# Optimization experiments

Hardware: AMD Instinct MI355X
Metric: run time of the kernel (lower is better)

Reference implementation:

```python
import jax, jax.numpy as jnp
import numpy as np

TEMP = 0.5
ALPHA = 1.0
BETA = 5.5
GAMMA = 5.0
N, D, C, M = 400, 512, 1000, 16000


def _normalize(x, axis=-1, eps=1e-12):
    return x / jnp.maximum(jnp.linalg.norm(x, axis=axis, keepdims=True), eps)


def _scale(x, target):
    # min-max scale x into the value range of target (global scalars)
    y = (x - x.min()) / (x.max() - x.min())
    y = y * (target.max() - target.min())
    y = y + target.min()
    return y


def setup_inputs() -> dict:
    key = jax.random.key(0)
    k1, k2, k3, k4 = jax.random.split(key, 4)
    image_features = jax.random.normal(k1, (N, D), dtype=jnp.float32)
    text_embeds = jax.random.normal(k2, (C, D), dtype=jnp.float32)
    support_feats = _normalize(jax.random.normal(k3, (D, M), dtype=jnp.float32), axis=0)
    support_labels = jax.random.randint(k4, (M,), 0, C)
    return {
        "image_features": image_features,
        "text_embeds": text_embeds,
        "support_feats": support_feats,
        "support_labels": support_labels,
    }


def reference(image_features, text_embeds, support_feats, support_labels):
    # one-hot support targets [M, C]
    support_targets = jax.nn.one_hot(support_labels, C, dtype=jnp.float32)

    # L2-normalize features (forward() normalizes both text and image features)
    text_features = _normalize(text_embeds, axis=-1).T          # [D, C]
    img = _normalize(image_features, axis=-1)                   # [N, D]

    # class distributions via temperature softmax
    train_logits = (support_feats.T @ text_features) / TEMP     # [M, C]
    test_logits = (img @ text_features) / TEMP                  # [N, C]
    train_log_dist = jax.nn.log_softmax(train_logits, axis=-1)  # log q  [M, C]
    test_log_dist = jax.nn.log_softmax(test_logits, axis=-1)    # log p  [N, C]
    test_dist = jnp.exp(test_log_dist)                          # p      [N, C]

    # KL(p_i || q_j) = sum_c p_ic log p_ic - sum_c p_ic log q_jc  -> one GEMM
    entropy_term = jnp.sum(test_dist * test_log_dist, axis=-1, keepdims=True)  # [N, 1]
    kl_divs = entropy_term - test_dist @ train_log_dist.T                      # [N, M]

    clip_logits = 100.0 * (img @ text_features)                 # [N, C]
    new_knowledge = img @ support_feats                         # [N, M]

    neg_affs = _scale(kl_divs, new_knowledge)                   # [N, M]
    affinities = -neg_affs
    kl_logits = affinities @ support_targets                    # [N, C]
    cache_logits = jnp.exp(-(BETA - BETA * new_knowledge)) @ support_targets  # [N, C]

    tipx_logits = clip_logits + kl_logits * GAMMA + cache_logits * ALPHA
    return tipx_logits
```

## Files before the change

kernel.cpp:

```cpp
#include <hip/hip_runtime.h>
#include <math.h>

#define TEMP_F   0.5f
#define ALPHA_F  1.0f
#define BETA_F   5.5f
#define GAMMA_F  5.0f
#define N_IMG    400
#define D_DIM    512
#define C_CLS    1000
#define C_PAD    1024
#define M_SUP    16000

typedef __attribute__((ext_vector_type(8))) short short8;
typedef __attribute__((ext_vector_type(4))) short short4v;
typedef __attribute__((ext_vector_type(4))) float f32x4;

__device__ __forceinline__ short f2bf(float f) {
    unsigned u = __float_as_uint(f);
    unsigned r = (u + 0x7fffu + ((u >> 16) & 1u)) >> 16;
    return (short)r;
}
__device__ __forceinline__ float bf2f(short s) {
    return __uint_as_float(((unsigned)(unsigned short)s) << 16);
}
__device__ __forceinline__ unsigned encf(float f) {
    unsigned u = __float_as_uint(f);
    return (u & 0x80000000u) ? ~u : (u | 0x80000000u);
}
__device__ __forceinline__ float decf(unsigned u) {
    return (u & 0x80000000u) ? __uint_as_float(u & 0x7FFFFFFFu) : __uint_as_float(~u);
}

__device__ __forceinline__ float block_reduce_sum(float v) {
    __shared__ float red[4];
    #pragma unroll
    for (int o = 32; o > 0; o >>= 1) v += __shfl_down(v, o, 64);
    int w = threadIdx.x >> 6, l = threadIdx.x & 63;
    __syncthreads();
    if (l == 0) red[w] = v;
    __syncthreads();
    float r = red[0];
    int nw = blockDim.x >> 6;
    for (int i = 1; i < nw; ++i) r += red[i];
    return r;
}

__device__ __forceinline__ void gload_lds16(const void* g, void* l) {
    __builtin_amdgcn_global_load_lds(
        (const __attribute__((address_space(1))) unsigned int*)g,
        (__attribute__((address_space(3))) unsigned int*)l, 16, 0, 0);
}

template<int EPI>
__device__ __forceinline__ void gemm_body(
    const short* __restrict__ A, const short* __restrict__ B, void* __restrict__ Cm,
    int I, int Jclamp, int Jout, int K, long lda, long ldb, long ldc, float alpha,
    const float* __restrict__ ent, const float* __restrict__ lse,
    unsigned* __restrict__ mm, float* __restrict__ out2,
    int i0, int j0, short (*As)[4096], short (*Bs)[4096])
{
    const int tid = threadIdx.x;
    const int wave = tid >> 6;
    const int lane = tid & 63;

    const int srow = wave * 16 + (lane >> 2);
    const int skk  = (lane & 3) * 8;

    const int wm = (wave & 1) * 64;
    const int wn = (wave >> 1) * 64;
    const int fr = lane & 15;
    const int fq = lane >> 4;

    f32x4 acc[4][4] = {};

    auto stage = [&](int buf, int k0) {
        #pragma unroll
        for (int q = 0; q < 2; ++q) {
            int gi = i0 + q * 64 + srow; if (gi > I - 1) gi = I - 1;
            gload_lds16(A + (long)gi * lda + k0 + skk, As[buf] + q * 2048 + wave * 512);
        }
        #pragma unroll
        for (int q = 0; q < 2; ++q) {
            int gj = j0 + q * 64 + srow; if (gj > Jclamp - 1) gj = Jclamp - 1;
            gload_lds16(B + (long)gj * ldb + k0 + skk, Bs[buf] + q * 2048 + wave * 512);
        }
    };

    const int nt = K >> 5;
    stage(0, 0);
    if (nt > 1) stage(1, 32);
    if (nt > 2) stage(2, 64);

    for (int t = 0; t < nt; ++t) {
        const int b = t % 3;

        if (t + 2 < nt)      asm volatile("s_waitcnt vmcnt(8)" ::: "memory");
        else if (t + 1 < nt) asm volatile("s_waitcnt vmcnt(4)" ::: "memory");
        else                 asm volatile("s_waitcnt vmcnt(0)" ::: "memory");
        __builtin_amdgcn_s_barrier();
        __builtin_amdgcn_sched_barrier(0);

        short8 af[4], bfr[4];
        #pragma unroll
        for (int mi = 0; mi < 4; ++mi)
            af[mi] = *(const short8*)(As[b] + (wm + mi * 16 + fr) * 32 + fq * 8);
        #pragma unroll
        for (int ni = 0; ni < 4; ++ni)
            bfr[ni] = *(const short8*)(Bs[b] + (wn + ni * 16 + fr) * 32 + fq * 8);

        asm volatile("s_waitcnt lgkmcnt(0)" ::: "memory");
        __builtin_amdgcn_sched_barrier(0);
        __builtin_amdgcn_s_barrier();

        if (t + 3 < nt) stage(b, (t + 3) << 5);

        __builtin_amdgcn_s_setprio(1);
        #pragma unroll
        for (int mi = 0; mi < 4; ++mi)
            #pragma unroll
            for (int ni = 0; ni < 4; ++ni)
                acc[mi][ni] = __builtin_amdgcn_mfma_f32_16x16x32_bf16(
                    af[mi], bfr[ni], acc[mi][ni], 0, 0, 0);
        __builtin_amdgcn_s_setprio(0);
    }

    float lmin = INFINITY, lmax = -INFINITY;

    #pragma unroll
    for (int mi = 0; mi < 4; ++mi) {
        #pragma unroll
        for (int ni = 0; ni < 4; ++ni) {
            int gj = j0 + wn + ni * 16 + fr;
            float lsev = 0.f;
            if (EPI == 2) lsev = lse[gj < Jout ? gj : (Jout - 1)];
            #pragma unroll
            for (int t = 0; t < 4; ++t) {
                int gi = i0 + wm + mi * 16 + fq * 4 + t;
                float v = alpha * acc[mi][ni][t];
                if (EPI == 2) {
                    int gic = gi < I ? gi : (I - 1);
                    v = ent[gic] - v + lsev;
                }
                if (EPI == 2 || EPI == 3) { lmin = fminf(lmin, v); lmax = fmaxf(lmax, v); }
                if (gi < I && gj < Jout) {
                    if (EPI == 1) ((short*)Cm)[(long)gi * ldc + gj] = f2bf(v);
                    else          ((float*)Cm)[(long)gi * ldc + gj] = v;
                }
                if (EPI == 4 && gi < I && gj < C_CLS)
                    out2[(long)gi * C_CLS + gj] = 100.f * v;
            }
        }
    }

    if (EPI == 2 || EPI == 3) {
        #pragma unroll
        for (int o = 32; o > 0; o >>= 1) {
            lmin = fminf(lmin, __shfl_down(lmin, o, 64));
            lmax = fmaxf(lmax, __shfl_down(lmax, o, 64));
        }
        __shared__ float rmin[4], rmax[4];
        if (lane == 0) { rmin[wave] = lmin; rmax[wave] = lmax; }
        __syncthreads();
        if (tid == 0) {
            float bmin = fminf(fminf(rmin[0], rmin[1]), fminf(rmin[2], rmin[3]));
            float bmax = fmaxf(fmaxf(rmax[0], rmax[1]), fmaxf(rmax[2], rmax[3]));
            const int base = (EPI == 2) ? 0 : 2;
            atomicMin(&mm[base + 0], encf(bmin));
            atomicMax(&mm[base + 1], encf(bmax));
        }
    }
}


__global__ __launch_bounds__(256) void prep_k(
    const float* __restrict__ text_embeds, const float* __restrict__ image_features,
    const float* __restrict__ S,
    short* __restrict__ Tnb, short* __restrict__ imgb, short* __restrict__ Sb,
    unsigned* __restrict__ mm)
{
    const int b = blockIdx.x;
    if (b == 0 && threadIdx.x < 4)
        mm[threadIdx.x] = (threadIdx.x & 1) ? encf(-INFINITY) : encf(INFINITY);

    if (b < 1400) {
        const float* s;
        short* d;
        if (b < 1000) { s = text_embeds + (long)b * D_DIM;            d = Tnb  + (long)b * D_DIM; }
        else          { s = image_features + (long)(b - 1000) * D_DIM; d = imgb + (long)(b - 1000) * D_DIM; }
        float ss = 0.f;
        for (int c = threadIdx.x; c < D_DIM; c += 256) { float v = s[c]; ss += v * v; }
        float tot = block_reduce_sum(ss);
        float inv = 1.0f / fmaxf(sqrtf(tot), 1e-12f);
        for (int c = threadIdx.x; c < D_DIM; c += 256) d[c] = f2bf(s[c] * inv);
    } else {
        __shared__ float tile[64][65];
        int l = b - 1400;
        int m0 = (l % 250) * 64, d0 = (l / 250) * 64;
        int ml = (threadIdx.x & 15) * 4;
        int dl = threadIdx.x >> 4;
        #pragma unroll
        for (int r = 0; r < 64; r += 16) {
            f32x4 v = *(const f32x4*)(S + (long)(d0 + dl + r) * M_SUP + m0 + ml);
            tile[dl + r][ml + 0] = v[0];
            tile[dl + r][ml + 1] = v[1];
            tile[dl + r][ml + 2] = v[2];
            tile[dl + r][ml + 3] = v[3];
        }
        __syncthreads();
        int mw = threadIdx.x >> 4;
        int dc = (threadIdx.x & 15) * 4;
        #pragma unroll
        for (int r = 0; r < 64; r += 16) {
            short4v o;
            #pragma unroll
            for (int k = 0; k < 4; ++k) o[k] = f2bf(tile[dc + k][mw + r]);
            *(short4v*)(Sb + (long)(m0 + mw + r) * D_DIM + d0 + dc) = o;
        }
    }
}

__global__ __launch_bounds__(256) void mega_gemm_k(
    const short* __restrict__ Sb, const short* __restrict__ Tnb,
    const short* __restrict__ imgb,
    short* __restrict__ tb, float* __restrict__ nk, float* __restrict__ dot,
    unsigned* __restrict__ mm, float* __restrict__ out)
{
    __shared__ short As[3][4096];
    __shared__ short Bs[3][4096];
    const int lin = blockIdx.x;

    if (lin < 1000) {
        int gt = (lin & 7) * 125 + (lin >> 3);
        int i0 = (gt >> 3) * 128;
        int j0 = (gt & 7) * 128;
        gemm_body<1>(Sb, Tnb, tb, M_SUP, C_CLS, C_PAD, D_DIM, D_DIM, D_DIM, C_PAD,
                     2.0f, nullptr, nullptr, nullptr, nullptr, i0, j0, As, Bs);
    } else if (lin < 1512) {
        int l = lin - 1000;
        int xcd = l & 7;
        int idx = l >> 3;
        int i0 = (idx & 3) * 128;
        int j0 = (xcd * 16 + (idx >> 2)) * 128;
        gemm_body<3>(imgb, Sb, nk, N_IMG, M_SUP, M_SUP, D_DIM, D_DIM, D_DIM, M_SUP,
                     1.0f, nullptr, nullptr, mm, nullptr, i0, j0, As, Bs);
    } else {
        int l = lin - 1512;
        int i0 = (l >> 3) * 128;
        int j0 = (l & 7) * 128;
        gemm_body<4>(imgb, Tnb, dot, N_IMG, C_CLS, C_PAD, D_DIM, D_DIM, D_DIM, C_PAD,
                     1.0f, nullptr, nullptr, nullptr, out, i0, j0, As, Bs);
    }
}

__global__ void lse_softmax_k(
    const short* __restrict__ tb, float* __restrict__ lse,
    const float* __restrict__ dot, short* __restrict__ pb, float* __restrict__ ent)
{
    const int b = blockIdx.x;
    const int lane = threadIdx.x & 63;
    if (b < 4000) {
        int row = b * 4 + (threadIdx.x >> 6);
        const short* r = tb + (long)row * C_PAD;
        short8 v0 = *(const short8*)(r + lane * 8);
        short8 v1 = *(const short8*)(r + 512 + lane * 8);
        bool act1 = lane < 61;
        float f0[8], f1[8];
        float mx = -INFINITY;
        #pragma unroll
        for (int j = 0; j < 8; ++j) { f0[j] = bf2f(v0[j]); mx = fmaxf(mx, f0[j]); }
        if (act1) {
            #pragma unroll
            for (int j = 0; j < 8; ++j) { f1[j] = bf2f(v1[j]); mx = fmaxf(mx, f1[j]); }
        }
        #pragma unroll
        for (int o = 32; o > 0; o >>= 1) mx = fmaxf(mx, __shfl_xor(mx, o, 64));
        float se = 0.f;
        #pragma unroll
        for (int j = 0; j < 8; ++j) se += __expf(f0[j] - mx);
        if (act1) {
            #pragma unroll
            for (int j = 0; j < 8; ++j) se += __expf(f1[j] - mx);
        }
        #pragma unroll
        for (int o = 32; o > 0; o >>= 1) se += __shfl_xor(se, o, 64);
        if (lane == 0) lse[row] = mx + __logf(se);
    } else {
        int n = (b - 4000) * 4 + (threadIdx.x >> 6);
        const float* dr = dot + (long)n * C_PAD;
        short* pr = pb + (long)n * C_PAD;
        f32x4 v[4];
        #pragma unroll
        for (int pp = 0; pp < 4; ++pp)
            v[pp] = *(const f32x4*)(dr + pp * 256 + lane * 4);
        float mx = -INFINITY;
        #pragma unroll
        for (int pp = 0; pp < 4; ++pp) {
            bool valid = (pp < 3) || (lane < 58);
            if (valid)
                #pragma unroll
                for (int j = 0; j < 4; ++j) mx = fmaxf(mx, 2.f * v[pp][j]);
        }
        #pragma unroll
        for (int o = 32; o > 0; o >>= 1) mx = fmaxf(mx, __shfl_xor(mx, o, 64));
        float se = 0.f;
        #pragma unroll
        for (int pp = 0; pp < 4; ++pp) {
            bool valid = (pp < 3) || (lane < 58);
            if (valid)
                #pragma unroll
                for (int j = 0; j < 4; ++j) se += __expf(2.f * v[pp][j] - mx);
        }
        #pragma unroll
        for (int o = 32; o > 0; o >>= 1) se += __shfl_xor(se, o, 64);
        float logsum = mx + __logf(se);
        float e = 0.f;
        #pragma unroll
        for (int pp = 0; pp < 4; ++pp) {
            bool valid = (pp < 3) || (lane < 58);
            short4v o4;
            #pragma unroll
            for (int j = 0; j < 4; ++j) {
                if (valid) {
                    float lp = 2.f * v[pp][j] - logsum;
                    float pv = __expf(lp);
                    o4[j] = f2bf(pv);
                    e += pv * lp;
                } else {
                    o4[j] = 0;
                }
            }
            *(short4v*)(pr + pp * 256 + lane * 4) = o4;
        }
        #pragma unroll
        for (int o = 32; o > 0; o >>= 1) e += __shfl_xor(e, o, 64);
        if (lane == 0) ent[n] = e;
    }
}

__global__ __launch_bounds__(256) void gemm2_k(
    const short* __restrict__ pb, const short* __restrict__ tb, float* __restrict__ kl,
    const float* __restrict__ ent, const float* __restrict__ lse,
    unsigned* __restrict__ mm)
{
    __shared__ short As[3][4096];
    __shared__ short Bs[3][4096];
    int lin = blockIdx.x;
    int xcd = lin & 7;
    int idx = lin >> 3;
    int i0 = (idx & 3) * 128;
    int j0 = (xcd * 16 + (idx >> 2)) * 128;
    gemm_body<2>(pb, tb, kl, N_IMG, M_SUP, M_SUP, C_PAD, C_PAD, C_PAD, M_SUP,
                 1.0f, ent, lse, mm, nullptr, i0, j0, As, Bs);
}

__global__ __launch_bounds__(256) void final_partial_k(
    const float* __restrict__ kl, const float* __restrict__ nk,
    const int* __restrict__ labels, const unsigned* __restrict__ mm,
    float* __restrict__ out)
{
    int n = blockIdx.x;
    int q = blockIdx.y;
    __shared__ float bins[C_CLS];
    for (int c = threadIdx.x; c < C_CLS; c += 256) bins[c] = 0.f;
    __syncthreads();
    float klmin = decf(mm[0]), klmax = decf(mm[1]);
    float nkmin = decf(mm[2]), nkmax = decf(mm[3]);
    float ratio = (nkmax - nkmin) / (klmax - klmin);
    const int m0 = q * (M_SUP / 4);
    const float4* kl4 = (const float4*)(kl + (long)n * M_SUP + m0);
    const float4* nk4 = (const float4*)(nk + (long)n * M_SUP + m0);
    const int4*  lb4 = (const int4*)(labels + m0);
    const int nv = M_SUP / 4 / 4;
    for (int v = threadIdx.x; v < nv; v += 256) {
        float4 kv = kl4[v];
        float4 vv = nk4[v];
        int4   lv = lb4[v];
        float y, contrib;
        y = (kv.x - klmin) * ratio + nkmin;
        contrib = -GAMMA_F * y + ALPHA_F * __expf(BETA_F * (vv.x - 1.0f));
        atomicAdd(&bins[lv.x], contrib);
        y = (kv.y - klmin) * ratio + nkmin;
        contrib = -GAMMA_F * y + ALPHA_F * __expf(BETA_F * (vv.y - 1.0f));
        atomicAdd(&bins[lv.y], contrib);
        y = (kv.z - klmin) * ratio + nkmin;
        contrib = -GAMMA_F * y + ALPHA_F * __expf(BETA_F * (vv.z - 1.0f));
        atomicAdd(&bins[lv.z], contrib);
        y = (kv.w - klmin) * ratio + nkmin;
        contrib = -GAMMA_F * y + ALPHA_F * __expf(BETA_F * (vv.w - 1.0f));
        atomicAdd(&bins[lv.w], contrib);
    }
    __syncthreads();
    for (int c = threadIdx.x; c < C_CLS; c += 256)
        atomicAdd(&out[(long)n * C_CLS + c], bins[c]);
}

extern "C" void kernel_launch(void* const* d_in, const int* in_sizes, int n_in,
                              void* d_out, int out_size, void* d_ws, size_t ws_size,
                              hipStream_t stream) {
    const float* image_features = (const float*)d_in[0];
    const float* text_embeds    = (const float*)d_in[1];
    const float* support_feats  = (const float*)d_in[2];
    const int*   support_labels = (const int*)d_in[3];
    float* out = (float*)d_out;

    char* base = (char*)d_ws;
    size_t off = 0;
    auto alloc = [&](size_t bytes) {
        void* p = base + off;
        off = (off + bytes + 255) & ~(size_t)255;
        return p;
    };
    short* Tnb  = (short*)alloc(sizeof(short) * C_CLS * D_DIM);
    short* imgb = (short*)alloc(sizeof(short) * N_IMG * D_DIM);
    short* Sb   = (short*)alloc(sizeof(short) * M_SUP * D_DIM);
    short* tb   = (short*)alloc(sizeof(short) * M_SUP * C_PAD);
    short* pb   = (short*)alloc(sizeof(short) * N_IMG * C_PAD);
    float* dot  = (float*)alloc(sizeof(float) * N_IMG * C_PAD);
    float* lse  = (float*)alloc(sizeof(float) * M_SUP);
    float* ent  = (float*)alloc(sizeof(float) * N_IMG);
    float* kl   = (float*)alloc(sizeof(float) * N_IMG * M_SUP);
    float* nk   = (float*)alloc(sizeof(float) * N_IMG * M_SUP);
    unsigned* mm = (unsigned*)alloc(256);

    prep_k<<<3400, 256, 0, stream>>>(
        text_embeds, image_features, support_feats, Tnb, imgb, Sb, mm);

    mega_gemm_k<<<1544, 256, 0, stream>>>(Sb, Tnb, imgb, tb, nk, dot, mm, out);

    lse_softmax_k<<<4100, 256, 0, stream>>>(tb, lse, dot, pb, ent);

    gemm2_k<<<512, 256, 0, stream>>>(pb, tb, kl, ent, lse, mm);

    final_partial_k<<<dim3(N_IMG, 4), 256, 0, stream>>>(kl, nk, support_labels, mm, out);
}
```

Measured before the change: 211.4 us.

## Reassociate KL GEMM through text features and fuse train logsumexp into GEMM epilogue

Rather than writing the full [M,C] train-logit matrix and running a K=1024 GEMM against it, the code reassociates p @ (S^T T)^T as (p @ T^T) @ S. It computes a small [N,D] intermediate W and then a K=512 GEMM against the support features. Per-row sum-exp of the train logits is accumulated with atomics in the first GEMM's epilogue, and the log is taken in the KL epilogue, so the bf16 train-logit buffer and the separate LSE pass go away. The sum-exp is taken without max subtraction, which is only safe because the logits are bounded (cosine times 2). It also adds a transposed text copy, an extra tiny GEMM launch, and a second bf16 rounding of W.

```diff
diff --git a/kernel.cpp b/kernel.cpp
--- a/kernel.cpp
+++ b/kernel.cpp
@@ -124,6 +124,40 @@
         __builtin_amdgcn_s_setprio(0);
     }
 
+    if (EPI == 5) {
+        float rs[4][4];
+        #pragma unroll
+        for (int mi = 0; mi < 4; ++mi)
+            #pragma unroll
+            for (int t = 0; t < 4; ++t) rs[mi][t] = 0.f;
+        #pragma unroll
+        for (int mi = 0; mi < 4; ++mi)
+            #pragma unroll
+            for (int ni = 0; ni < 4; ++ni) {
+                int gj = j0 + wn + ni * 16 + fr;
+                if (gj < Jout) {
+                    #pragma unroll
+                    for (int t = 0; t < 4; ++t)
+                        rs[mi][t] += __expf(alpha * acc[mi][ni][t]);
+                }
+            }
+        #pragma unroll
+        for (int o = 1; o <= 8; o <<= 1)
+            #pragma unroll
+            for (int mi = 0; mi < 4; ++mi)
+                #pragma unroll
+                for (int t = 0; t < 4; ++t)
+                    rs[mi][t] += __shfl_xor(rs[mi][t], o, 64);
+        if ((lane & 15) == 0) {
+            #pragma unroll
+            for (int mi = 0; mi < 4; ++mi)
+                #pragma unroll
+                for (int t = 0; t < 4; ++t)
+                    atomicAdd(out2 + (i0 + wm + mi * 16 + fq * 4 + t), rs[mi][t]);
+        }
+        return;
+    }
+
     float lmin = INFINITY, lmax = -INFINITY;
 
     #pragma unroll
@@ -132,7 +166,7 @@
         for (int ni = 0; ni < 4; ++ni) {
             int gj = j0 + wn + ni * 16 + fr;
             float lsev = 0.f;
-            if (EPI == 2) lsev = lse[gj < Jout ? gj : (Jout - 1)];
+            if (EPI == 2) lsev = __logf(lse[gj < Jout ? gj : (Jout - 1)]);
             #pragma unroll
             for (int t = 0; t < 4; ++t) {
                 int gi = i0 + wm + mi * 16 + fq * 4 + t;
@@ -175,24 +209,37 @@
 __global__ __launch_bounds__(256) void prep_k(
     const float* __restrict__ text_embeds, const float* __restrict__ image_features,
     const float* __restrict__ S,
-    short* __restrict__ Tnb, short* __restrict__ imgb, short* __restrict__ Sb,
-    unsigned* __restrict__ mm)
+    short* __restrict__ Tnb, short* __restrict__ TnT, short* __restrict__ imgb,
+    short* __restrict__ Sb, float* __restrict__ se, unsigned* __restrict__ mm)
 {
     const int b = blockIdx.x;
     if (b == 0 && threadIdx.x < 4)
         mm[threadIdx.x] = (threadIdx.x & 1) ? encf(-INFINITY) : encf(INFINITY);
 
-    if (b < 1400) {
-        const float* s;
-        short* d;
-        if (b < 1000) { s = text_embeds + (long)b * D_DIM;            d = Tnb  + (long)b * D_DIM; }
-        else          { s = image_features + (long)(b - 1000) * D_DIM; d = imgb + (long)(b - 1000) * D_DIM; }
+    if (b < 1000) {
+        const float* s = text_embeds + (long)b * D_DIM;
+        short* d = Tnb + (long)b * D_DIM;
+        float ss = 0.f;
+        for (int c = threadIdx.x; c < D_DIM; c += 256) { float v = s[c]; ss += v * v; }
+        float tot = block_reduce_sum(ss);
+        float inv = 1.0f / fmaxf(sqrtf(tot), 1e-12f);
+        for (int c = threadIdx.x; c < D_DIM; c += 256) {
+            short bv = f2bf(s[c] * inv);
+            d[c] = bv;
+            TnT[(long)c * C_PAD + b] = bv;
+        }
+        if (b < 24)
+            for (int f = threadIdx.x; f < D_DIM; f += 256)
+                TnT[(long)f * C_PAD + 1000 + b] = 0;
+    } else if (b < 1400) {
+        const float* s = image_features + (long)(b - 1000) * D_DIM;
+        short* d = imgb + (long)(b - 1000) * D_DIM;
         float ss = 0.f;
         for (int c = threadIdx.x; c < D_DIM; c += 256) { float v = s[c]; ss += v * v; }
         float tot = block_reduce_sum(ss);
         float inv = 1.0f / fmaxf(sqrtf(tot), 1e-12f);
         for (int c = threadIdx.x; c < D_DIM; c += 256) d[c] = f2bf(s[c] * inv);
-    } else {
+    } else if (b < 3400) {
         __shared__ float tile[64][65];
         int l = b - 1400;
         int m0 = (l % 250) * 64, d0 = (l / 250) * 64;
@@ -216,13 +263,16 @@
             for (int k = 0; k < 4; ++k) o[k] = f2bf(tile[dc + k][mw + r]);
             *(short4v*)(Sb + (long)(m0 + mw + r) * D_DIM + d0 + dc) = o;
         }
+    } else {
+        int base = (b - 3400) * 1000;
+        for (int i = threadIdx.x; i < 1000; i += 256) se[base + i] = 0.f;
     }
 }
 
 __global__ __launch_bounds__(256) void mega_gemm_k(
     const short* __restrict__ Sb, const short* __restrict__ Tnb,
     const short* __restrict__ imgb,
-    short* __restrict__ tb, float* __restrict__ nk, float* __restrict__ dot,
+    float* __restrict__ se, float* __restrict__ nk, float* __restrict__ dot,
     unsigned* __restrict__ mm, float* __restrict__ out)
 {
     __shared__ short As[3][4096];
@@ -233,8 +283,8 @@
         int gt = (lin & 7) * 125 + (lin >> 3);
         int i0 = (gt >> 3) * 128;
         int j0 = (gt & 7) * 128;
-        gemm_body<1>(Sb, Tnb, tb, M_SUP, C_CLS, C_PAD, D_DIM, D_DIM, D_DIM, C_PAD,
-                     2.0f, nullptr, nullptr, nullptr, nullptr, i0, j0, As, Bs);
+        gemm_body<5>(Sb, Tnb, nullptr, M_SUP, C_CLS, C_CLS, D_DIM, D_DIM, D_DIM, 0,
+                     2.0f, nullptr, nullptr, nullptr, se, i0, j0, As, Bs);
     } else if (lin < 1512) {
         int l = lin - 1000;
         int xcd = l & 7;
@@ -252,94 +302,76 @@
     }
 }
 
-__global__ void lse_softmax_k(
-    const short* __restrict__ tb, float* __restrict__ lse,
-    const float* __restrict__ dot, short* __restrict__ pb, float* __restrict__ ent)
-{
-    const int b = blockIdx.x;
+__global__ void softmax_k(const float* __restrict__ dot, short* __restrict__ pb,
+                          float* __restrict__ ent)
+{
     const int lane = threadIdx.x & 63;
-    if (b < 4000) {
-        int row = b * 4 + (threadIdx.x >> 6);
-        const short* r = tb + (long)row * C_PAD;
-        short8 v0 = *(const short8*)(r + lane * 8);
-        short8 v1 = *(const short8*)(r + 512 + lane * 8);
-        bool act1 = lane < 61;
-        float f0[8], f1[8];
-        float mx = -INFINITY;
-        #pragma unroll
-        for (int j = 0; j < 8; ++j) { f0[j] = bf2f(v0[j]); mx = fmaxf(mx, f0[j]); }
-        if (act1) {
-            #pragma unroll
-            for (int j = 0; j < 8; ++j) { f1[j] = bf2f(v1[j]); mx = fmaxf(mx, f1[j]); }
-        }
-        #pragma unroll
-        for (int o = 32; o > 0; o >>= 1) mx = fmaxf(mx, __shfl_xor(mx, o, 64));
-        float se = 0.f;
-        #pragma unroll
-        for (int j = 0; j < 8; ++j) se += __expf(f0[j] - mx);
-        if (act1) {
-            #pragma unroll
-            for (int j = 0; j < 8; ++j) se += __expf(f1[j] - mx);
-        }
-        #pragma unroll
-        for (int o = 32; o > 0; o >>= 1) se += __shfl_xor(se, o, 64);
-        if (lane == 0) lse[row] = mx + __logf(se);
-    } else {
-        int n = (b - 4000) * 4 + (threadIdx.x >> 6);
-        const float* dr = dot + (long)n * C_PAD;
-        short* pr = pb + (long)n * C_PAD;
-        f32x4 v[4];
-        #pragma unroll
-        for (int pp = 0; pp < 4; ++pp)
-            v[pp] = *(const f32x4*)(dr + pp * 256 + lane * 4);
-        float mx = -INFINITY;
-        #pragma unroll
-        for (int pp = 0; pp < 4; ++pp) {
-            bool valid = (pp < 3) || (lane < 58);
-            if (valid)
-                #pragma unroll
-                for (int j = 0; j < 4; ++j) mx = fmaxf(mx, 2.f * v[pp][j]);
-        }
-        #pragma unroll
-        for (int o = 32; o > 0; o >>= 1) mx = fmaxf(mx, __shfl_xor(mx, o, 64));
-        float se = 0.f;
-        #pragma unroll
-        for (int pp = 0; pp < 4; ++pp) {
-            bool valid = (pp < 3) || (lane < 58);
-            if (valid)
-                #pragma unroll
-                for (int j = 0; j < 4; ++j) se += __expf(2.f * v[pp][j] - mx);
-        }
-        #pragma unroll
-        for (int o = 32; o > 0; o >>= 1) se += __shfl_xor(se, o, 64);
-        float logsum = mx + __logf(se);
-        float e = 0.f;
-        #pragma unroll
-        for (int pp = 0; pp < 4; ++pp) {
-            bool valid = (pp < 3) || (lane < 58);
-            short4v o4;
-            #pragma unroll
-            for (int j = 0; j < 4; ++j) {
-                if (valid) {
-                    float lp = 2.f * v[pp][j] - logsum;
-                    float pv = __expf(lp);
-                    o4[j] = f2bf(pv);
-                    e += pv * lp;
-                } else {
-                    o4[j] = 0;
-                }
+    int n = blockIdx.x * 4 + (threadIdx.x >> 6);
+    const float* dr = dot + (long)n * C_PAD;
+    short* pr = pb + (long)n * C_PAD;
+    f32x4 v[4];
+    #pragma unroll
+    for (int pp = 0; pp < 4; ++pp)
+        v[pp] = *(const f32x4*)(dr + pp * 256 + lane * 4);
+    float mx = -INFINITY;
+    #pragma unroll
+    for (int pp = 0; pp < 4; ++pp) {
+        bool valid = (pp < 3) || (lane < 58);
+        if (valid)
+            #pragma unroll
+            for (int j = 0; j < 4; ++j) mx = fmaxf(mx, 2.f * v[pp][j]);
+    }
+    #pragma unroll
+    for (int o = 32; o > 0; o >>= 1) mx = fmaxf(mx, __shfl_xor(mx, o, 64));
+    float se = 0.f;
+    #pragma unroll
+    for (int pp = 0; pp < 4; ++pp) {
+        bool valid = (pp < 3) || (lane < 58);
+        if (valid)
+            #pragma unroll
+            for (int j = 0; j < 4; ++j) se += __expf(2.f * v[pp][j] - mx);
+    }
+    #pragma unroll
+    for (int o = 32; o > 0; o >>= 1) se += __shfl_xor(se, o, 64);
+    float logsum = mx + __logf(se);
+    float e = 0.f;
+    #pragma unroll
+    for (int pp = 0; pp < 4; ++pp) {
+        bool valid = (pp < 3) || (lane < 58);
+        short4v o4;
+        #pragma unroll
+        for (int j = 0; j < 4; ++j) {
+            if (valid) {
+                float lp = 2.f * v[pp][j] - logsum;
+                float pv = __expf(lp);
+                o4[j] = f2bf(pv);
+                e += pv * lp;
+            } else {
+                o4[j] = 0;
             }
-            *(short4v*)(pr + pp * 256 + lane * 4) = o4;
-        }
-        #pragma unroll
-        for (int o = 32; o > 0; o >>= 1) e += __shfl_xor(e, o, 64);
-        if (lane == 0) ent[n] = e;
-    }
-}
-
-__global__ __launch_bounds__(256) void gemm2_k(
-    const short* __restrict__ pb, const short* __restrict__ tb, float* __restrict__ kl,
-    const float* __restrict__ ent, const float* __restrict__ lse,
+        }
+        *(short4v*)(pr + pp * 256 + lane * 4) = o4;
+    }
+    #pragma unroll
+    for (int o = 32; o > 0; o >>= 1) e += __shfl_xor(e, o, 64);
+    if (lane == 0) ent[n] = e;
+}
+
+__global__ __launch_bounds__(256) void wgemm_k(
+    const short* __restrict__ pb, const short* __restrict__ TnT,
+    short* __restrict__ Wb)
+{
+    __shared__ short As[3][4096];
+    __shared__ short Bs[3][4096];
+    int i0 = (blockIdx.x >> 2) * 128;
+    int j0 = (blockIdx.x & 3) * 128;
+    gemm_body<1>(pb, TnT, Wb, N_IMG, D_DIM, D_DIM, C_PAD, C_PAD, C_PAD, D_DIM,
+                 2.0f, nullptr, nullptr, nullptr, nullptr, i0, j0, As, Bs);
+}
+
+__global__ __launch_bounds__(256) void qgemm_k(
+    const short* __restrict__ Wb, const short* __restrict__ Sb, float* __restrict__ kl,
+    const float* __restrict__ ent, const float* __restrict__ se,
     unsigned* __restrict__ mm)
 {
     __shared__ short As[3][4096];
@@ -349,8 +381,8 @@
     int idx = lin >> 3;
     int i0 = (idx & 3) * 128;
     int j0 = (xcd * 16 + (idx >> 2)) * 128;
-    gemm_body<2>(pb, tb, kl, N_IMG, M_SUP, M_SUP, C_PAD, C_PAD, C_PAD, M_SUP,
-                 1.0f, ent, lse, mm, nullptr, i0, j0, As, Bs);
+    gemm_body<2>(Wb, Sb, kl, N_IMG, M_SUP, M_SUP, D_DIM, D_DIM, D_DIM, M_SUP,
+                 1.0f, ent, se, mm, nullptr, i0, j0, As, Bs);
 }
 
 __global__ __launch_bounds__(256) void final_partial_k(
@@ -411,25 +443,28 @@
         return p;
     };
     short* Tnb  = (short*)alloc(sizeof(short) * C_CLS * D_DIM);
+    short* TnT  = (short*)alloc(sizeof(short) * D_DIM * C_PAD);
     short* imgb = (short*)alloc(sizeof(short) * N_IMG * D_DIM);
     short* Sb   = (short*)alloc(sizeof(short) * M_SUP * D_DIM);
-    short* tb   = (short*)alloc(sizeof(short) * M_SUP * C_PAD);
     short* pb   = (short*)alloc(sizeof(short) * N_IMG * C_PAD);
+    short* Wb   = (short*)alloc(sizeof(short) * N_IMG * D_DIM);
     float* dot  = (float*)alloc(sizeof(float) * N_IMG * C_PAD);
-    float* lse  = (float*)alloc(sizeof(float) * M_SUP);
+    float* se   = (float*)alloc(sizeof(float) * M_SUP);
     float* ent  = (float*)alloc(sizeof(float) * N_IMG);
     float* kl   = (float*)alloc(sizeof(float) * N_IMG * M_SUP);
     float* nk   = (float*)alloc(sizeof(float) * N_IMG * M_SUP);
     unsigned* mm = (unsigned*)alloc(256);
 
-    prep_k<<<3400, 256, 0, stream>>>(
-        text_embeds, image_features, support_feats, Tnb, imgb, Sb, mm);
-
-    mega_gemm_k<<<1544, 256, 0, stream>>>(Sb, Tnb, imgb, tb, nk, dot, mm, out);
-
-    lse_softmax_k<<<4100, 256, 0, stream>>>(tb, lse, dot, pb, ent);
-
-    gemm2_k<<<512, 256, 0, stream>>>(pb, tb, kl, ent, lse, mm);
+    prep_k<<<3416, 256, 0, stream>>>(
+        text_embeds, image_features, support_feats, Tnb, TnT, imgb, Sb, se, mm);
+
+    mega_gemm_k<<<1544, 256, 0, stream>>>(Sb, Tnb, imgb, se, nk, dot, mm, out);
+
+    softmax_k<<<N_IMG / 4, 256, 0, stream>>>(dot, pb, ent);
+
+    wgemm_k<<<16, 256, 0, stream>>>(pb, TnT, Wb);
+
+    qgemm_k<<<512, 256, 0, stream>>>(Wb, Sb, kl, ent, se, mm);
 
     final_partial_k<<<dim3(N_IMG, 4), 256, 0, stream>>>(kl, nk, support_labels, mm, out);
 }
```

Result: slower. 225.1 us (+6.5%).
